# Performance work log

Measured on AMD Instinct MI355X. Metric: run time of the kernel, lower is better.

## Reference

```python
import jax, jax.numpy as jnp
import numpy as np

N, M = 4096, 8192
IN_DIM, OUT_DIM = 4096, 1024
NUM_SAMPLE = 10


def setup_inputs() -> dict:
    key = jax.random.key(0)
    k1, k2, k3, k4, k5 = jax.random.split(key, 5)
    node_features = jax.random.normal(k1, (N, IN_DIM), dtype=jnp.float32)
    neighbor_features = jax.random.normal(k2, (M, IN_DIM), dtype=jnp.float32)
    # Xavier-ish scale for params
    weight = jax.random.normal(k3, (OUT_DIM, IN_DIM), dtype=jnp.float32) * (1.0 / np.sqrt(IN_DIM))
    attention_vector = jax.random.normal(k4, (2 * OUT_DIM, 1), dtype=jnp.float32) * 0.05
    neighbor_idx = jax.random.randint(k5, (N, NUM_SAMPLE), 0, M, dtype=jnp.int32)
    return {
        "node_features": node_features,
        "neighbor_features": neighbor_features,
        "weight": weight,
        "attention_vector": attention_vector,
        "neighbor_idx": neighbor_idx,
    }


def reference(node_features, neighbor_features, weight, attention_vector, neighbor_idx):
    # Linear transform: [N, out], [M, out]
    node_t = node_features @ weight.T
    neigh_t = neighbor_features @ weight.T

    # combined @ attention_vector decomposes:
    # cat([h_i, h_j]) @ a == h_i @ a1 + h_j @ a2  (same math, no [N,M,2*out] tensor)
    a1 = attention_vector[:OUT_DIM, 0]   # [out]
    a2 = attention_vector[OUT_DIM:, 0]   # [out]
    scores = jax.nn.leaky_relu((node_t @ a1)[:, None] + (neigh_t @ a2)[None, :],
                               negative_slope=0.2)  # [N, M]

    # Build dense 0/1 mask from sampled neighbor indices (ragged -> dense)
    rows = jnp.arange(N, dtype=jnp.int32)[:, None]                  # [N,1]
    mask = jnp.zeros((N, M), dtype=jnp.float32).at[rows, neighbor_idx].set(1.0)

    scores = jnp.where(mask == 0, -jnp.inf, scores)
    attn = jax.nn.softmax(scores, axis=1)           # masked softmax over neighbor pool
    return attn @ neigh_t                           # [N, out]
```

## Files before the change

kernel.cpp:

```cpp
#include <hip/hip_runtime.h>

#define IN_DIM  4096
#define OUT_DIM 1024
#define NN      4096
#define MM      8192
#define NSAMP   10

typedef __bf16 bf16x8 __attribute__((ext_vector_type(8)));
typedef float  fx4    __attribute__((ext_vector_type(4)));

__device__ __forceinline__ ushort f2bf(float f) {
    union { float f; unsigned u; } v; v.f = f;
    unsigned u = v.u;
    return (ushort)((u + 0x7FFFu + ((u >> 16) & 1u)) >> 16);
}

__global__ __launch_bounds__(256) void k_attvec(const float* __restrict__ W,
                                                const float* __restrict__ att,
                                                float* __restrict__ v1,
                                                float* __restrict__ v2) {
    int k  = blockIdx.x * 256 + threadIdx.x;
    int o0 = blockIdx.y * 128;
    float s1 = 0.f, s2 = 0.f;
    for (int o = o0; o < o0 + 128; ++o) {
        float w = W[(size_t)o * IN_DIM + k];
        s1 += att[o] * w;
        s2 += att[OUT_DIM + o] * w;
    }
    atomicAdd(&v1[k], s1);
    atomicAdd(&v2[k], s2);
}

__global__ __launch_bounds__(256) void k_node_alpha(const float* __restrict__ X,
                                                    const float* __restrict__ v1,
                                                    float* __restrict__ outv) {
    int row = blockIdx.x;
    const float4* xr = reinterpret_cast<const float4*>(X + (size_t)row * IN_DIM);
    const float4* vr = reinterpret_cast<const float4*>(v1);
    float s = 0.f;
    for (int i = threadIdx.x; i < IN_DIM / 4; i += 256) {
        float4 a = xr[i], b = vr[i];
        s += a.x * b.x + a.y * b.y + a.z * b.z + a.w * b.w;
    }
    for (int off = 32; off > 0; off >>= 1) s += __shfl_down(s, off, 64);
    __shared__ float ws[4];
    if ((threadIdx.x & 63) == 0) ws[threadIdx.x >> 6] = s;
    __syncthreads();
    if (threadIdx.x == 0) outv[row] = ws[0] + ws[1] + ws[2] + ws[3];
}

__global__ __launch_bounds__(256) void k_cast_beta(const float* __restrict__ X,
                                                   const float* __restrict__ v2,
                                                   ushort* __restrict__ Xbf,
                                                   float* __restrict__ beta) {
    int row = blockIdx.x;
    const float4* xr = reinterpret_cast<const float4*>(X + (size_t)row * IN_DIM);
    const float4* vr = reinterpret_cast<const float4*>(v2);
    ushort4* yr = reinterpret_cast<ushort4*>(Xbf + (size_t)row * IN_DIM);
    float s = 0.f;
    for (int i = threadIdx.x; i < IN_DIM / 4; i += 256) {
        float4 a = xr[i], b = vr[i];
        s += a.x * b.x + a.y * b.y + a.z * b.z + a.w * b.w;
        ushort4 o;
        o.x = f2bf(a.x); o.y = f2bf(a.y); o.z = f2bf(a.z); o.w = f2bf(a.w);
        yr[i] = o;
    }
    for (int off = 32; off > 0; off >>= 1) s += __shfl_down(s, off, 64);
    __shared__ float ws[4];
    if ((threadIdx.x & 63) == 0) ws[threadIdx.x >> 6] = s;
    __syncthreads();
    if (threadIdx.x == 0) beta[row] = ws[0] + ws[1] + ws[2] + ws[3];
}

__global__ __launch_bounds__(256) void k_cast(const float* __restrict__ X,
                                              ushort* __restrict__ Y, int n4) {
    int i = blockIdx.x * blockDim.x + threadIdx.x;
    int stride = gridDim.x * blockDim.x;
    for (; i < n4; i += stride) {
        float4 a = reinterpret_cast<const float4*>(X)[i];
        ushort4 o;
        o.x = f2bf(a.x); o.y = f2bf(a.y); o.z = f2bf(a.z); o.w = f2bf(a.w);
        reinterpret_cast<ushort4*>(Y)[i] = o;
    }
}

#define TM   128
#define TN   128
#define BK   32
#define LDSW 40

__global__ __launch_bounds__(256) void k_gemm(const ushort* __restrict__ A,
                                              const ushort* __restrict__ B,
                                              float* __restrict__ C) {
    __shared__ __align__(16) ushort As[TM * LDSW];
    __shared__ __align__(16) ushort Bs[TN * LDSW];
    const int tid  = threadIdx.x;
    const int lane = tid & 63;
    const int wave = tid >> 6;
    const int wm   = (wave >> 1) * 64;
    const int wn   = (wave & 1) * 64;
    const int bm   = blockIdx.x * TM;
    const int bn   = blockIdx.y * TN;
    const int quad = lane >> 4;
    const int lrow = lane & 15;
    const int sr   = tid >> 2;
    const int sc   = (tid & 3) * 8;

    fx4 acc[4][4] = {};

    for (int k0 = 0; k0 < IN_DIM; k0 += BK) {
        uint4 a0 = *reinterpret_cast<const uint4*>(A + (size_t)(bm + sr)      * IN_DIM + k0 + sc);
        uint4 a1 = *reinterpret_cast<const uint4*>(A + (size_t)(bm + sr + 64) * IN_DIM + k0 + sc);
        uint4 b0 = *reinterpret_cast<const uint4*>(B + (size_t)(bn + sr)      * IN_DIM + k0 + sc);
        uint4 b1 = *reinterpret_cast<const uint4*>(B + (size_t)(bn + sr + 64) * IN_DIM + k0 + sc);
        *reinterpret_cast<uint4*>(As + sr * LDSW + sc)        = a0;
        *reinterpret_cast<uint4*>(As + (sr + 64) * LDSW + sc) = a1;
        *reinterpret_cast<uint4*>(Bs + sr * LDSW + sc)        = b0;
        *reinterpret_cast<uint4*>(Bs + (sr + 64) * LDSW + sc) = b1;
        __syncthreads();

        bf16x8 af[4], bf[4];
#pragma unroll
        for (int mi = 0; mi < 4; ++mi)
            af[mi] = *reinterpret_cast<const bf16x8*>(As + (wm + mi * 16 + lrow) * LDSW + quad * 8);
#pragma unroll
        for (int ni = 0; ni < 4; ++ni)
            bf[ni] = *reinterpret_cast<const bf16x8*>(Bs + (wn + ni * 16 + lrow) * LDSW + quad * 8);
#pragma unroll
        for (int mi = 0; mi < 4; ++mi)
#pragma unroll
            for (int ni = 0; ni < 4; ++ni)
                acc[mi][ni] = __builtin_amdgcn_mfma_f32_16x16x32_bf16(af[mi], bf[ni], acc[mi][ni], 0, 0, 0);
        __syncthreads();
    }

#pragma unroll
    for (int mi = 0; mi < 4; ++mi)
#pragma unroll
        for (int ni = 0; ni < 4; ++ni) {
            int r = bm + wm + mi * 16 + quad * 4;
            int c = bn + wn + ni * 16 + lrow;
#pragma unroll
            for (int v = 0; v < 4; ++v)
                C[(size_t)(r + v) * OUT_DIM + c] = acc[mi][ni][v];
        }
}

__global__ __launch_bounds__(256) void k_aggregate(const float* __restrict__ neigh_t,
                                                   const float* __restrict__ nalpha,
                                                   const float* __restrict__ nbeta,
                                                   const int* __restrict__ nidx,
                                                   float* __restrict__ outp) {
    int row = blockIdx.x;
    __shared__ int   s_idx[NSAMP];
    __shared__ float s_w[NSAMP];
    __shared__ int   s_cnt;
    if (threadIdx.x == 0) {
        int   tmp[NSAMP];
        float sc[NSAMP];
        int   cnt = 0;
        float alpha = nalpha[row];
        float mx = -INFINITY;
        for (int s = 0; s < NSAMP; ++s) {
            int j = nidx[row * NSAMP + s];
            bool dup = false;
            for (int t = 0; t < cnt; ++t)
                if (tmp[t] == j) { dup = true; break; }
            if (!dup) {
                float x = alpha + nbeta[j];
                float v = x > 0.f ? x : 0.2f * x;
                tmp[cnt] = j;
                sc[cnt] = v;
                if (v > mx) mx = v;
                ++cnt;
            }
        }
        float sum = 0.f;
        for (int t = 0; t < cnt; ++t) { float e = expf(sc[t] - mx); sc[t] = e; sum += e; }
        float inv = 1.f / sum;
        for (int t = 0; t < cnt; ++t) { s_idx[t] = tmp[t]; s_w[t] = sc[t] * inv; }
        s_cnt = cnt;
    }
    __syncthreads();
    int cnt = s_cnt;
    int col = threadIdx.x * 4;
    float ax = 0.f, ay = 0.f, az = 0.f, aw = 0.f;
    for (int t = 0; t < cnt; ++t) {
        float w = s_w[t];
        float4 v = *reinterpret_cast<const float4*>(neigh_t + (size_t)s_idx[t] * OUT_DIM + col);
        ax += w * v.x; ay += w * v.y; az += w * v.z; aw += w * v.w;
    }
    float4 o; o.x = ax; o.y = ay; o.z = az; o.w = aw;
    *reinterpret_cast<float4*>(outp + (size_t)row * OUT_DIM + col) = o;
}

extern "C" void kernel_launch(void* const* d_in, const int* in_sizes, int n_in,
                              void* d_out, int out_size, void* d_ws, size_t ws_size,
                              hipStream_t stream) {
    const float* node_f  = (const float*)d_in[0];
    const float* neigh_f = (const float*)d_in[1];
    const float* W       = (const float*)d_in[2];
    const float* att     = (const float*)d_in[3];
    const int*   nidx    = (const int*)d_in[4];
    float* outp = (float*)d_out;

    char* ws = (char*)d_ws;
    ushort* Abf     = (ushort*)ws;
    ushort* Wbf     = (ushort*)(ws + 67108864);
    float*  neigh_t = (float*)(ws + 75497472);
    float*  v1      = (float*)(ws + 109051904);
    float*  v2      = v1 + IN_DIM;
    float*  nalpha  = v2 + IN_DIM;
    float*  nbeta   = nalpha + NN;

    hipMemsetAsync(v1, 0, 2 * IN_DIM * sizeof(float), stream);

    k_attvec    <<<dim3(16, 8), 256, 0, stream>>>(W, att, v1, v2);
    k_node_alpha<<<NN,          256, 0, stream>>>(node_f, v1, nalpha);
    k_cast_beta <<<MM,          256, 0, stream>>>(neigh_f, v2, Abf, nbeta);
    k_cast      <<<1024,        256, 0, stream>>>(W, Wbf, OUT_DIM * IN_DIM / 4);
    k_gemm      <<<dim3(MM / TM, OUT_DIM / TN), 256, 0, stream>>>(Abf, Wbf, neigh_t);
    k_aggregate <<<NN,          256, 0, stream>>>(neigh_t, nalpha, nbeta, nidx, outp);
}
```

Baseline: 407.9 us.

## Fuse weight bf16 cast into attvec and stage GEMM tiles via global-load-LDS

The weight-to-bf16 conversion now happens inside the attention-vector kernel, which already reads W. This drops a separate cast launch and a second read of W. The GEMM now loads A/B tiles directly into LDS with global_load_lds instead of going through registers, and the LDS tiles lose their padding. Without padding, the fragment reads may hit LDS bank conflicts.

```diff
diff --git a/kernel.cpp b/kernel.cpp
--- a/kernel.cpp
+++ b/kernel.cpp
@@ -15,15 +15,21 @@
     return (ushort)((u + 0x7FFFu + ((u >> 16) & 1u)) >> 16);
 }
 
+#define GLDS(g, l) __builtin_amdgcn_global_load_lds(                           \
+    (const __attribute__((address_space(1))) unsigned*)(g),                    \
+    (__attribute__((address_space(3))) unsigned*)(l), 16, 0, 0)
+
 __global__ __launch_bounds__(256) void k_attvec(const float* __restrict__ W,
                                                 const float* __restrict__ att,
                                                 float* __restrict__ v1,
-                                                float* __restrict__ v2) {
+                                                float* __restrict__ v2,
+                                                ushort* __restrict__ Wbf) {
     int k  = blockIdx.x * 256 + threadIdx.x;
     int o0 = blockIdx.y * 128;
     float s1 = 0.f, s2 = 0.f;
     for (int o = o0; o < o0 + 128; ++o) {
         float w = W[(size_t)o * IN_DIM + k];
+        Wbf[(size_t)o * IN_DIM + k] = f2bf(w);
         s1 += att[o] * w;
         s2 += att[OUT_DIM + o] * w;
     }
@@ -72,28 +78,15 @@
     if (threadIdx.x == 0) beta[row] = ws[0] + ws[1] + ws[2] + ws[3];
 }
 
-__global__ __launch_bounds__(256) void k_cast(const float* __restrict__ X,
-                                              ushort* __restrict__ Y, int n4) {
-    int i = blockIdx.x * blockDim.x + threadIdx.x;
-    int stride = gridDim.x * blockDim.x;
-    for (; i < n4; i += stride) {
-        float4 a = reinterpret_cast<const float4*>(X)[i];
-        ushort4 o;
-        o.x = f2bf(a.x); o.y = f2bf(a.y); o.z = f2bf(a.z); o.w = f2bf(a.w);
-        reinterpret_cast<ushort4*>(Y)[i] = o;
-    }
-}
-
-#define TM   128
-#define TN   128
-#define BK   32
-#define LDSW 40
+#define TM 128
+#define TN 128
+#define BK 32
 
 __global__ __launch_bounds__(256) void k_gemm(const ushort* __restrict__ A,
                                               const ushort* __restrict__ B,
                                               float* __restrict__ C) {
-    __shared__ __align__(16) ushort As[TM * LDSW];
-    __shared__ __align__(16) ushort Bs[TN * LDSW];
+    __shared__ __align__(16) ushort As[TM * BK];
+    __shared__ __align__(16) ushort Bs[TN * BK];
     const int tid  = threadIdx.x;
     const int lane = tid & 63;
     const int wave = tid >> 6;
@@ -103,34 +96,35 @@
     const int bn   = blockIdx.y * TN;
     const int quad = lane >> 4;
     const int lrow = lane & 15;
-    const int sr   = tid >> 2;
-    const int sc   = (tid & 3) * 8;
+
+    const int srow  = wave * 32 + (lane >> 2);
+    const int skoff = (lane & 3) * 8;
+    const ushort* gA = A + (size_t)(bm + srow) * IN_DIM + skoff;
+    const ushort* gB = B + (size_t)(bn + srow) * IN_DIM + skoff;
+    ushort* lA = As + wave * 1024;
+    ushort* lB = Bs + wave * 1024;
 
     fx4 acc[4][4] = {};
 
     for (int k0 = 0; k0 < IN_DIM; k0 += BK) {
-        uint4 a0 = *reinterpret_cast<const uint4*>(A + (size_t)(bm + sr)      * IN_DIM + k0 + sc);
-        uint4 a1 = *reinterpret_cast<const uint4*>(A + (size_t)(bm + sr + 64) * IN_DIM + k0 + sc);
-        uint4 b0 = *reinterpret_cast<const uint4*>(B + (size_t)(bn + sr)      * IN_DIM + k0 + sc);
-        uint4 b1 = *reinterpret_cast<const uint4*>(B + (size_t)(bn + sr + 64) * IN_DIM + k0 + sc);
-        *reinterpret_cast<uint4*>(As + sr * LDSW + sc)        = a0;
-        *reinterpret_cast<uint4*>(As + (sr + 64) * LDSW + sc) = a1;
-        *reinterpret_cast<uint4*>(Bs + sr * LDSW + sc)        = b0;
-        *reinterpret_cast<uint4*>(Bs + (sr + 64) * LDSW + sc) = b1;
+        GLDS(gA + k0,                lA);
+        GLDS(gA + k0 + 16 * IN_DIM,  lA + 512);
+        GLDS(gB + k0,                lB);
+        GLDS(gB + k0 + 16 * IN_DIM,  lB + 512);
         __syncthreads();
 
-        bf16x8 af[4], bf[4];
+        bf16x8 af[4], bfr[4];
 #pragma unroll
         for (int mi = 0; mi < 4; ++mi)
-            af[mi] = *reinterpret_cast<const bf16x8*>(As + (wm + mi * 16 + lrow) * LDSW + quad * 8);
+            af[mi] = *reinterpret_cast<const bf16x8*>(As + (wm + mi * 16 + lrow) * BK + quad * 8);
 #pragma unroll
         for (int ni = 0; ni < 4; ++ni)
-            bf[ni] = *reinterpret_cast<const bf16x8*>(Bs + (wn + ni * 16 + lrow) * LDSW + quad * 8);
+            bfr[ni] = *reinterpret_cast<const bf16x8*>(Bs + (wn + ni * 16 + lrow) * BK + quad * 8);
 #pragma unroll
         for (int mi = 0; mi < 4; ++mi)
 #pragma unroll
             for (int ni = 0; ni < 4; ++ni)
-                acc[mi][ni] = __builtin_amdgcn_mfma_f32_16x16x32_bf16(af[mi], bf[ni], acc[mi][ni], 0, 0, 0);
+                acc[mi][ni] = __builtin_amdgcn_mfma_f32_16x16x32_bf16(af[mi], bfr[ni], acc[mi][ni], 0, 0, 0);
         __syncthreads();
     }
 
@@ -215,10 +209,9 @@
 
     hipMemsetAsync(v1, 0, 2 * IN_DIM * sizeof(float), stream);
 
-    k_attvec    <<<dim3(16, 8), 256, 0, stream>>>(W, att, v1, v2);
+    k_attvec    <<<dim3(16, 8), 256, 0, stream>>>(W, att, v1, v2, Wbf);
     k_node_alpha<<<NN,          256, 0, stream>>>(node_f, v1, nalpha);
     k_cast_beta <<<MM,          256, 0, stream>>>(neigh_f, v2, Abf, nbeta);
-    k_cast      <<<1024,        256, 0, stream>>>(W, Wbf, OUT_DIM * IN_DIM / 4);
     k_gemm      <<<dim3(MM / TM, OUT_DIM / TN), 256, 0, stream>>>(Abf, Wbf, neigh_t);
     k_aggregate <<<NN,          256, 0, stream>>>(neigh_t, nalpha, nbeta, nidx, outp);
 }
```

After: 438.9 us. +7.6%, slower.
